# Performance work log

Hardware: AMD Instinct MI355X
Metric: run time of the kernel (lower is better)

Reference implementation:

```python
import jax, jax.numpy as jnp
import numpy as np
import math

BATCH, SEQ, D_MODEL, HEADS = 2, 2048, 1024, 16
DK = D_MODEL // HEADS  # 64
THETA = 10000.0


def _init_linear(key, d_in, d_out):
    std = math.sqrt(2.0 / (d_in + d_out))
    return (jax.random.truncated_normal(key, -3.0, 3.0, (d_in, d_out), jnp.float32) * std)


def setup_inputs() -> dict:
    key = jax.random.key(0)
    kx, kq, kk, kv, ko = jax.random.split(key, 5)
    x = jax.random.normal(kx, (BATCH, SEQ, D_MODEL), jnp.float32)
    W_Q = _init_linear(kq, D_MODEL, D_MODEL)
    W_K = _init_linear(kk, D_MODEL, D_MODEL)
    W_V = _init_linear(kv, D_MODEL, D_MODEL)
    W_O = _init_linear(ko, D_MODEL, D_MODEL)
    token_positions = jnp.arange(SEQ, dtype=jnp.int64 if jax.config.jax_enable_x64 else jnp.int32)
    # RoPE tables: angle[i, k] = i / theta**(2k/d_k), shape [max_seq_len, d_k//2]
    pos = jnp.arange(SEQ, dtype=jnp.float32)[:, None]
    inv_freq = THETA ** (-2.0 * jnp.arange(DK // 2, dtype=jnp.float32) / DK)
    angles = pos * inv_freq
    return {
        "x": x,
        "token_positions": token_positions,
        "W_Q": W_Q,
        "W_K": W_K,
        "W_V": W_V,
        "W_O": W_O,
        "cos": jnp.cos(angles),
        "sin": jnp.sin(angles),
    }


def _apply_rope(t, cos_p, sin_p):
    # t: [B, H, S, DK]; cos_p/sin_p: [S, DK//2] (already gathered by position)
    t_even = t[..., 0::2]
    t_odd = t[..., 1::2]
    even_rot = cos_p * t_even - sin_p * t_odd
    odd_rot = sin_p * t_even + cos_p * t_odd
    # interleave back: [..., DK//2, 2] -> [..., DK]
    return jnp.stack([even_rot, odd_rot], axis=-1).reshape(t.shape)


def reference(x, token_positions, W_Q, W_K, W_V, W_O, cos, sin):
    B, S, D = x.shape
    H, dk = HEADS, D // HEADS
    # QKV projections, split into heads: [B, S, D] -> [B, H, S, dk]
    def proj(W):
        return jnp.einsum("bsd,de->bse", x, W).reshape(B, S, H, dk).transpose(0, 2, 1, 3)
    Q, K, V = proj(W_Q), proj(W_K), proj(W_V)
    cos_p = cos[token_positions]  # [S, dk//2]
    sin_p = sin[token_positions]
    Q = _apply_rope(Q, cos_p, sin_p)
    K = _apply_rope(K, cos_p, sin_p)
    scores = jnp.einsum("bhqd,bhkd->bhqk", Q, K) / jnp.sqrt(jnp.asarray(dk, x.dtype))
    causal = jnp.tril(jnp.ones((S, S), dtype=bool))
    scores = jnp.where(causal, scores, -jnp.inf)
    attn = jax.nn.softmax(scores, axis=-1)
    out = jnp.einsum("bhqk,bhkd->bhqd", attn, V)  # [B, H, S, dk]
    out = out.transpose(0, 2, 1, 3).reshape(B, S, D)
    return jnp.einsum("bsd,de->bse", out, W_O)
```

## Files before the change

kernel.cpp:

```cpp
#include <hip/hip_runtime.h>

typedef unsigned short u16;
typedef unsigned int   u32;
typedef __bf16  bf16x8 __attribute__((ext_vector_type(8)));
typedef float   f32x4  __attribute__((ext_vector_type(4)));
typedef u32     u32x4  __attribute__((ext_vector_type(4)));

#define SEQ    2048
#define HEADS  16
#define DM     1024
#define NBH    32
#define NBS    4096

__device__ __forceinline__ u16 f2b(float f) {
    u32 x;
    __builtin_memcpy(&x, &f, 4);
    return (u16)((x + 0x7fffu + ((x >> 16) & 1u)) >> 16);
}

__device__ __forceinline__ u32 pk2(float lo, float hi) {
    return (u32)f2b(lo) | ((u32)f2b(hi) << 16);
}

__device__ __forceinline__ u32 pkc(float lo, float hi) {
    __bf16 a = (__bf16)lo, b = (__bf16)hi;
    u16 x, y;
    __builtin_memcpy(&x, &a, 2);
    __builtin_memcpy(&y, &b, 2);
    return (u32)x | ((u32)y << 16);
}

__device__ __forceinline__ bf16x8 ld_bf8(const u16* p) {
    return *(const bf16x8*)p;
}
__device__ __forceinline__ bf16x8 ld_f32x8_cvt(const float* p) {
    f32x4 a = *(const f32x4*)p;
    f32x4 b = *(const f32x4*)(p + 4);
    bf16x8 r;
    r[0] = (__bf16)a[0]; r[1] = (__bf16)a[1]; r[2] = (__bf16)a[2]; r[3] = (__bf16)a[3];
    r[4] = (__bf16)b[0]; r[5] = (__bf16)b[1]; r[6] = (__bf16)b[2]; r[7] = (__bf16)b[3];
    return r;
}

__global__ __launch_bounds__(256) void transpose_wqkv(const float* __restrict__ Wq,
                                                      const float* __restrict__ Wk,
                                                      const float* __restrict__ Wv,
                                                      u16* __restrict__ WqkvT) {
    __shared__ u16 tile[64][65];
    const int z  = blockIdx.z;
    const float* src = (z == 0) ? Wq : (z == 1) ? Wk : Wv;
    const int k0 = blockIdx.x * 64, n0 = blockIdx.y * 64;
    const int tid = threadIdx.x;
    for (int i = 0; i < 16; ++i) {
        int e = i * 256 + tid;
        int r = e >> 6, c = e & 63;
        tile[r][c] = f2b(src[(size_t)(k0 + r) * DM + n0 + c]);
    }
    __syncthreads();
    u16* dst = WqkvT + (size_t)z * DM * DM;
    for (int i = 0; i < 16; ++i) {
        int e = i * 256 + tid;
        int r = e >> 6, c = e & 63;
        dst[(size_t)(n0 + r) * DM + k0 + c] = tile[c][r];
    }
}

__global__ __launch_bounds__(256) void transpose_wo(const float* __restrict__ Wo,
                                                    u16* __restrict__ WoT) {
    __shared__ u16 tile[64][65];
    const int k0 = blockIdx.x * 64, n0 = blockIdx.y * 64;
    const int tid = threadIdx.x;
    for (int i = 0; i < 16; ++i) {
        int e = i * 256 + tid;
        int r = e >> 6, c = e & 63;
        tile[r][c] = f2b(Wo[(size_t)(k0 + r) * DM + n0 + c]);
    }
    __syncthreads();
    for (int i = 0; i < 16; ++i) {
        int e = i * 256 + tid;
        int r = e >> 6, c = e & 63;
        WoT[(size_t)(n0 + r) * DM + k0 + c] = tile[c][r];
    }
}

#define GEMM_BODY(A_EXPR, B_EXPR, K)                                                \
    __shared__ __attribute__((aligned(16))) __bf16 As[128 * 64];                    \
    __shared__ __attribute__((aligned(16))) __bf16 Bs[128 * 64];                    \
    const int tid  = threadIdx.x;                                                   \
    const int wave = tid >> 6, lane = tid & 63;                                     \
    const int quad = lane >> 4, col = lane & 15;                                    \
    const int wm = wave >> 1, wn = wave & 1;                                        \
    const int m0 = blockIdx.x * 128, n0 = blockIdx.y * 128;                         \
    const int srow = tid >> 3;                                           \
    const int scol = (tid & 7) * 8;                                      \
    f32x4 zero = {0.f, 0.f, 0.f, 0.f};                                              \
    f32x4 acc[4][4];                                                                \
    for (int i = 0; i < 4; ++i)                                                     \
        for (int j = 0; j < 4; ++j) acc[i][j] = zero;                               \
    for (int k0 = 0; k0 < (K); k0 += 64) {                                          \
        bf16x8 av[4], bv[4];                                                        \
        for (int p = 0; p < 4; ++p) {                                               \
            int row = p * 32 + srow;                                                \
            av[p] = A_EXPR;                                                         \
            bv[p] = B_EXPR;                                                         \
        }                                                                           \
        __syncthreads();                                                            \
        for (int p = 0; p < 4; ++p) {                                               \
            int row = p * 32 + srow;                                                \
            *(bf16x8*)&As[row * 64 + scol] = av[p];                                 \
            *(bf16x8*)&Bs[row * 64 + scol] = bv[p];                                 \
        }                                                                           \
        __syncthreads();                                                            \
        for (int ks = 0; ks < 2; ++ks) {                                            \
            bf16x8 af[4], bfr[4];                                                   \
            for (int mt = 0; mt < 4; ++mt)                                          \
                af[mt] = *(const bf16x8*)&As[(wm * 64 + mt * 16 + col) * 64 +       \
                                             ks * 32 + quad * 8];                   \
            for (int nt = 0; nt < 4; ++nt)                                          \
                bfr[nt] = *(const bf16x8*)&Bs[(wn * 64 + nt * 16 + col) * 64 +      \
                                              ks * 32 + quad * 8];                  \
            for (int mt = 0; mt < 4; ++mt)                                          \
                for (int nt = 0; nt < 4; ++nt)                                      \
                    acc[mt][nt] = __builtin_amdgcn_mfma_f32_16x16x32_bf16(          \
                        af[mt], bfr[nt], acc[mt][nt], 0, 0, 0);                     \
        }                                                                           \
    }

__global__ __launch_bounds__(256) void gemm_qkv(const float* __restrict__ Af,
                                                const u16* __restrict__ Bt,
                                                u16* __restrict__ Qp,
                                                u16* __restrict__ Kp,
                                                u16* __restrict__ Vt) {
    GEMM_BODY(ld_f32x8_cvt(Af + (size_t)(m0 + row) * DM + k0 + scol),
              ld_bf8(Bt + (size_t)(n0 + row) * DM + k0 + scol), DM)
    for (int mt = 0; mt < 4; ++mt)
        for (int nt = 0; nt < 4; ++nt) {
            int cc = n0 + wn * 64 + nt * 16 + col;
            int which = cc >> 10;
            int c1 = cc & 1023;
            int h = c1 >> 6, d = c1 & 63;
            for (int r = 0; r < 4; ++r) {
                int row = m0 + wm * 64 + mt * 16 + quad * 4 + r;
                int b = row >> 11, s = row & (SEQ - 1);
                u16 val = f2b(acc[mt][nt][r]);
                size_t bh = (size_t)(b * HEADS + h);
                if (which == 0)
                    Qp[(bh * SEQ + s) * 64 + d] = val;
                else if (which == 1)
                    Kp[(bh * SEQ + s) * 64 + d] = val;
                else
                    Vt[(bh * 64 + d) * SEQ + s] = val;
            }
        }
}

__global__ __launch_bounds__(256) void gemm_wo(const u16* __restrict__ A,
                                               const u16* __restrict__ Bt,
                                               float* __restrict__ C) {
    GEMM_BODY(ld_bf8(A + (size_t)(m0 + row) * DM + k0 + scol),
              ld_bf8(Bt + (size_t)(n0 + row) * DM + k0 + scol), DM)
    for (int mt = 0; mt < 4; ++mt)
        for (int nt = 0; nt < 4; ++nt)
            for (int r = 0; r < 4; ++r) {
                int row = m0 + wm * 64 + mt * 16 + quad * 4 + r;
                int cc  = n0 + wn * 64 + nt * 16 + col;
                C[(size_t)row * DM + cc] = acc[mt][nt][r];
            }
}

__global__ __launch_bounds__(256) void rope_qk(u16* __restrict__ Qp,
                                               u16* __restrict__ Kp,
                                               const float* __restrict__ cosT,
                                               const float* __restrict__ sinT) {
    int t = blockIdx.x * 256 + threadIdx.x;
    int p  = t & 31;
    int s  = (t >> 5) & (SEQ - 1);
    int hh = (t >> 16) & (HEADS - 1);
    int b  = t >> 20;

    float cv = cosT[s * 32 + p];
    float sv = sinT[s * 32 + p];

    size_t addr = (((size_t)(b * HEADS + hh)) * SEQ + s) * 64 + 2 * p;
    u32 q2 = *(const u32*)(Qp + addr);
    u32 k2 = *(const u32*)(Kp + addr);
    u32 qe_b = (q2 & 0xffff) << 16, qo_b = q2 & 0xffff0000u;
    u32 ke_b = (k2 & 0xffff) << 16, ko_b = k2 & 0xffff0000u;
    float qe, qo, ke, ko;
    __builtin_memcpy(&qe, &qe_b, 4); __builtin_memcpy(&qo, &qo_b, 4);
    __builtin_memcpy(&ke, &ke_b, 4); __builtin_memcpy(&ko, &ko_b, 4);

    u32 qout = (u32)f2b(0.125f * (cv * qe - sv * qo)) |
               ((u32)f2b(0.125f * (sv * qe + cv * qo)) << 16);
    u32 kout = (u32)f2b(cv * ke - sv * ko) | ((u32)f2b(sv * ke + cv * ko) << 16);
    *(u32*)(Qp + addr) = qout;
    *(u32*)(Kp + addr) = kout;
}

__global__ __launch_bounds__(256, 3) void flash_attn(const u16* __restrict__ Qp,
                                                     const u16* __restrict__ Kp,
                                                     const u16* __restrict__ Vt,
                                                     u16* __restrict__ O) {
    __shared__ float os[4][32][68];
    __shared__ float mM[4][32];
    __shared__ float mL[4][32];
    const int tid  = threadIdx.x;
    const int wave = tid >> 6, lane = tid & 63;
    const int quad = lane >> 4, col = lane & 15;
    const bool hi5 = lane >= 32;
    const bool hi4 = (lane & 16) != 0;
    const int bh = blockIdx.x;
    const int b = bh >> 4, h = bh & 15;
    const int qt = 63 - blockIdx.y;
    const int q0 = qt * 32;

    const u16* Qb = Qp + (size_t)bh * SEQ * 64;
    const u16* Kb = Kp + (size_t)bh * SEQ * 64;
    const u16* Vb = Vt + (size_t)bh * 64 * SEQ;

    bf16x8 bq00 = ld_bf8(Qb + (size_t)(q0 + col) * 64 + quad * 8);
    bf16x8 bq01 = ld_bf8(Qb + (size_t)(q0 + col) * 64 + 32 + quad * 8);
    bf16x8 bq10 = ld_bf8(Qb + (size_t)(q0 + 16 + col) * 64 + quad * 8);
    bf16x8 bq11 = ld_bf8(Qb + (size_t)(q0 + 16 + col) * 64 + 32 + quad * 8);

    f32x4 zero = {0.f, 0.f, 0.f, 0.f};
    f32x4 o0[4] = {zero, zero, zero, zero};
    f32x4 o1[4] = {zero, zero, zero, zero};
    float m0_ = -1e30f, m1_ = -1e30f;
    float lp0 = 0.f, lp1 = 0.f;

    const int nkt = qt + 1;
    int kt = wave;
    bf16x8 ck00, ck01, ck10, ck11;
    if (kt < nkt) {
        const int kb = kt << 5;
        ck00 = ld_bf8(Kb + (size_t)(kb + col) * 64 + quad * 8);
        ck01 = ld_bf8(Kb + (size_t)(kb + col) * 64 + 32 + quad * 8);
        ck10 = ld_bf8(Kb + (size_t)(kb + 16 + col) * 64 + quad * 8);
        ck11 = ld_bf8(Kb + (size_t)(kb + 16 + col) * 64 + 32 + quad * 8);
    }

    for (; kt < nkt; kt += 4) {
        const int kb = kt << 5;
        bf16x8 bv0 = ld_bf8(Vb + (size_t)(0 * 16 + col) * SEQ + kb + quad * 8);
        bf16x8 bv1 = ld_bf8(Vb + (size_t)(1 * 16 + col) * SEQ + kb + quad * 8);
        bf16x8 bv2 = ld_bf8(Vb + (size_t)(2 * 16 + col) * SEQ + kb + quad * 8);
        bf16x8 bv3 = ld_bf8(Vb + (size_t)(3 * 16 + col) * SEQ + kb + quad * 8);
        int kn = kt + 4; if (kn >= nkt) kn = kt;
        const int kb2 = kn << 5;
        bf16x8 nk00 = ld_bf8(Kb + (size_t)(kb2 + col) * 64 + quad * 8);
        bf16x8 nk01 = ld_bf8(Kb + (size_t)(kb2 + col) * 64 + 32 + quad * 8);
        bf16x8 nk10 = ld_bf8(Kb + (size_t)(kb2 + 16 + col) * 64 + quad * 8);
        bf16x8 nk11 = ld_bf8(Kb + (size_t)(kb2 + 16 + col) * 64 + 32 + quad * 8);

        f32x4 s00 = zero, s01 = zero, s10 = zero, s11 = zero;
        s00 = __builtin_amdgcn_mfma_f32_16x16x32_bf16(ck00, bq00, s00, 0, 0, 0);
        s10 = __builtin_amdgcn_mfma_f32_16x16x32_bf16(ck00, bq10, s10, 0, 0, 0);
        s00 = __builtin_amdgcn_mfma_f32_16x16x32_bf16(ck01, bq01, s00, 0, 0, 0);
        s10 = __builtin_amdgcn_mfma_f32_16x16x32_bf16(ck01, bq11, s10, 0, 0, 0);
        s01 = __builtin_amdgcn_mfma_f32_16x16x32_bf16(ck10, bq00, s01, 0, 0, 0);
        s11 = __builtin_amdgcn_mfma_f32_16x16x32_bf16(ck10, bq10, s11, 0, 0, 0);
        s01 = __builtin_amdgcn_mfma_f32_16x16x32_bf16(ck11, bq01, s01, 0, 0, 0);
        s11 = __builtin_amdgcn_mfma_f32_16x16x32_bf16(ck11, bq11, s11, 0, 0, 0);

        float v00[4], v01[4], v10[4], v11[4];
        float lm0 = -1e30f, lm1 = -1e30f;
        if (kt == qt) {
            for (int r = 0; r < 4; ++r) {
                int krel = quad * 4 + r;
                float a0 = (krel > col) ? -1e30f : s00[r];
                float b0 = -1e30f;
                float a1 = s10[r];
                float b1 = (krel > col) ? -1e30f : s11[r];
                v00[r] = a0; v01[r] = b0; v10[r] = a1; v11[r] = b1;
                lm0 = fmaxf(lm0, fmaxf(a0, b0));
                lm1 = fmaxf(lm1, fmaxf(a1, b1));
            }
        } else {
            for (int r = 0; r < 4; ++r) {
                v00[r] = s00[r]; v01[r] = s01[r];
                v10[r] = s10[r]; v11[r] = s11[r];
                lm0 = fmaxf(lm0, fmaxf(v00[r], v01[r]));
                lm1 = fmaxf(lm1, fmaxf(v10[r], v11[r]));
            }
        }

        float dd = fmaxf(lm0 - m0_, lm1 - m1_);
        if (__any(dd > 8.f)) {
            float lr0 = fmaxf(lm0, __shfl_xor(lm0, 16));
            lr0 = fmaxf(lr0, __shfl_xor(lr0, 32));
            float lr1 = fmaxf(lm1, __shfl_xor(lm1, 16));
            lr1 = fmaxf(lr1, __shfl_xor(lr1, 32));
            float mn0 = fmaxf(m0_, lr0), mn1 = fmaxf(m1_, lr1);
            float al0 = __expf(m0_ - mn0), al1 = __expf(m1_ - mn1);
            m0_ = mn0; m1_ = mn1;
            lp0 *= al0; lp1 *= al1;
            for (int r = 0; r < 4; ++r) {
                float ar0 = __shfl(al0, quad * 4 + r);
                float ar1 = __shfl(al1, quad * 4 + r);
                for (int nt = 0; nt < 4; ++nt) {
                    o0[nt][r] *= ar0;
                    o1[nt][r] *= ar1;
                }
            }
        }

        for (int r = 0; r < 4; ++r) {
            v00[r] = __expf(v00[r] - m0_);
            v01[r] = __expf(v01[r] - m0_);
            v10[r] = __expf(v10[r] - m1_);
            v11[r] = __expf(v11[r] - m1_);
            lp0 += v00[r] + v01[r];
            lp1 += v10[r] + v11[r];
        }

        u32 fwa0[4], fwa1[4];
        {
            u32 A0 = pkc(v00[0], v00[1]), A1 = pkc(v00[2], v00[3]);
            u32 B0 = pkc(v01[0], v01[1]), B1 = pkc(v01[2], v01[3]);
            u32 g0 = hi5 ? A0 : B0,  g1 = hi5 ? A1 : B1;
            u32 r0 = __shfl_xor(g0, 32), r1 = __shfl_xor(g1, 32);
            u32 P00 = hi5 ? r0 : A0,  P01 = hi5 ? r1 : A1;
            u32 P10 = hi5 ? B0 : r0,  P11 = hi5 ? B1 : r1;
            u32 h0 = hi4 ? P00 : P10, h1 = hi4 ? P01 : P11;
            u32 u0 = __shfl_xor(h0, 16), u1 = __shfl_xor(h1, 16);
            fwa0[0] = hi4 ? u0 : P00;  fwa0[1] = hi4 ? u1 : P01;
            fwa0[2] = hi4 ? P10 : u0;  fwa0[3] = hi4 ? P11 : u1;
        }
        {
            u32 A0 = pkc(v10[0], v10[1]), A1 = pkc(v10[2], v10[3]);
            u32 B0 = pkc(v11[0], v11[1]), B1 = pkc(v11[2], v11[3]);
            u32 g0 = hi5 ? A0 : B0,  g1 = hi5 ? A1 : B1;
            u32 r0 = __shfl_xor(g0, 32), r1 = __shfl_xor(g1, 32);
            u32 P00 = hi5 ? r0 : A0,  P01 = hi5 ? r1 : A1;
            u32 P10 = hi5 ? B0 : r0,  P11 = hi5 ? B1 : r1;
            u32 h0 = hi4 ? P00 : P10, h1 = hi4 ? P01 : P11;
            u32 u0 = __shfl_xor(h0, 16), u1 = __shfl_xor(h1, 16);
            fwa1[0] = hi4 ? u0 : P00;  fwa1[1] = hi4 ? u1 : P01;
            fwa1[2] = hi4 ? P10 : u0;  fwa1[3] = hi4 ? P11 : u1;
        }
        bf16x8 pf0, pf1;
        __builtin_memcpy(&pf0, fwa0, 16);
        __builtin_memcpy(&pf1, fwa1, 16);

        o0[0] = __builtin_amdgcn_mfma_f32_16x16x32_bf16(pf0, bv0, o0[0], 0, 0, 0);
        o1[0] = __builtin_amdgcn_mfma_f32_16x16x32_bf16(pf1, bv0, o1[0], 0, 0, 0);
        o0[1] = __builtin_amdgcn_mfma_f32_16x16x32_bf16(pf0, bv1, o0[1], 0, 0, 0);
        o1[1] = __builtin_amdgcn_mfma_f32_16x16x32_bf16(pf1, bv1, o1[1], 0, 0, 0);
        o0[2] = __builtin_amdgcn_mfma_f32_16x16x32_bf16(pf0, bv2, o0[2], 0, 0, 0);
        o1[2] = __builtin_amdgcn_mfma_f32_16x16x32_bf16(pf1, bv2, o1[2], 0, 0, 0);
        o0[3] = __builtin_amdgcn_mfma_f32_16x16x32_bf16(pf0, bv3, o0[3], 0, 0, 0);
        o1[3] = __builtin_amdgcn_mfma_f32_16x16x32_bf16(pf1, bv3, o1[3], 0, 0, 0);

        ck00 = nk00; ck01 = nk01; ck10 = nk10; ck11 = nk11;
    }

    float lt0 = lp0;
    lt0 += __shfl_xor(lt0, 16); lt0 += __shfl_xor(lt0, 32);
    float lt1 = lp1;
    lt1 += __shfl_xor(lt1, 16); lt1 += __shfl_xor(lt1, 32);
    if (quad == 0) {
        mM[wave][col] = m0_;      mL[wave][col] = lt0;
        mM[wave][16 + col] = m1_; mL[wave][16 + col] = lt1;
    }
    for (int nt = 0; nt < 4; ++nt)
        for (int r = 0; r < 4; ++r) {
            os[wave][quad * 4 + r][nt * 16 + col]      = o0[nt][r];
            os[wave][16 + quad * 4 + r][nt * 16 + col] = o1[nt][r];
        }
    __syncthreads();

    {
        const int q  = tid >> 3;
        const int d0 = (tid & 7) * 8;
        float M = fmaxf(fmaxf(mM[0][q], mM[1][q]), fmaxf(mM[2][q], mM[3][q]));
        float L = 0.f;
        f32x4 a0 = {0.f, 0.f, 0.f, 0.f}, a1 = {0.f, 0.f, 0.f, 0.f};
        for (int w = 0; w < 4; ++w) {
            float e = __expf(mM[w][q] - M);
            L += e * mL[w][q];
            f32x4 p0 = *(const f32x4*)&os[w][q][d0];
            f32x4 p1 = *(const f32x4*)&os[w][q][d0 + 4];
            for (int j = 0; j < 4; ++j) { a0[j] += e * p0[j]; a1[j] += e * p1[j]; }
        }
        float inv = 1.f / L;
        u32x4 val;
        val[0] = pk2(a0[0] * inv, a0[1] * inv);
        val[1] = pk2(a0[2] * inv, a0[3] * inv);
        val[2] = pk2(a1[0] * inv, a1[1] * inv);
        val[3] = pk2(a1[2] * inv, a1[3] * inv);
        *(u32x4*)&O[((size_t)b * SEQ + q0 + q) * DM + h * 64 + d0] = val;
    }
}

extern "C" void kernel_launch(void* const* d_in, const int* in_sizes, int n_in,
                              void* d_out, int out_size, void* d_ws, size_t ws_size,
                              hipStream_t stream) {
    const float* x    = (const float*)d_in[0];
    const float* Wq   = (const float*)d_in[2];
    const float* Wk   = (const float*)d_in[3];
    const float* Wv   = (const float*)d_in[4];
    const float* Wo   = (const float*)d_in[5];
    const float* cosT = (const float*)d_in[6];
    const float* sinT = (const float*)d_in[7];
    float* out = (float*)d_out;

    u16* ws    = (u16*)d_ws;
    u16* qp    = ws;
    u16* kp    = ws + 4194304;
    u16* vt    = ws + 8388608;
    u16* woT   = ws + 8388608;
    u16* wqkvT = ws + 12582912;
    u16* ao    = ws + 12582912;

    dim3 blk(256);
    transpose_wqkv<<<dim3(16, 16, 3), blk, 0, stream>>>(Wq, Wk, Wv, wqkvT);
    gemm_qkv<<<dim3(32, 24), blk, 0, stream>>>(x, wqkvT, qp, kp, vt);
    rope_qk<<<dim3(8192), blk, 0, stream>>>(qp, kp, cosT, sinT);
    flash_attn<<<dim3(NBH, 64), blk, 0, stream>>>(qp, kp, vt, ao);
    transpose_wo<<<dim3(16, 16), blk, 0, stream>>>(Wo, woT);
    gemm_wo<<<dim3(32, 8), blk, 0, stream>>>(ao, woT, out);
}
```

Measured before the change: 247.7 us.

## Use direct global-to-LDS loads with XOR swizzle in GEMMs and vectorize RoPE

Replaces the GEMM macro with explicit kernels that load bf16 tiles straight into LDS via global_load_lds and use an XOR-swizzled LDS layout to avoid bank conflicts on fragment reads. In gemm_qkv the fp32 activation tile for the next k-step is prefetched into registers while the current step computes. The RoPE kernel now processes 8 elements per thread with 128-bit loads and stores instead of 2. This cuts register staging and LDS conflicts, but the swizzle index math must stay consistent between writes and reads, and the direct-to-LDS path depends on the compiler builtin's semantics.

```diff
diff --git a/kernel.cpp b/kernel.cpp
--- a/kernel.cpp
+++ b/kernel.cpp
@@ -40,6 +40,13 @@
     r[0] = (__bf16)a[0]; r[1] = (__bf16)a[1]; r[2] = (__bf16)a[2]; r[3] = (__bf16)a[3];
     r[4] = (__bf16)b[0]; r[5] = (__bf16)b[1]; r[6] = (__bf16)b[2]; r[7] = (__bf16)b[3];
     return r;
+}
+
+__device__ __forceinline__ void gl_lds16(const u16* g, __bf16* l) {
+    __builtin_amdgcn_global_load_lds(
+        (__attribute__((address_space(1))) void*)g,
+        (__attribute__((address_space(3))) void*)l,
+        16, 0, 0);
 }
 
 __global__ __launch_bounds__(256) void transpose_wqkv(const float* __restrict__ Wq,
@@ -83,56 +90,67 @@
     }
 }
 
-#define GEMM_BODY(A_EXPR, B_EXPR, K)                                                \
-    __shared__ __attribute__((aligned(16))) __bf16 As[128 * 64];                    \
-    __shared__ __attribute__((aligned(16))) __bf16 Bs[128 * 64];                    \
-    const int tid  = threadIdx.x;                                                   \
-    const int wave = tid >> 6, lane = tid & 63;                                     \
-    const int quad = lane >> 4, col = lane & 15;                                    \
-    const int wm = wave >> 1, wn = wave & 1;                                        \
-    const int m0 = blockIdx.x * 128, n0 = blockIdx.y * 128;                         \
-    const int srow = tid >> 3;                                           \
-    const int scol = (tid & 7) * 8;                                      \
-    f32x4 zero = {0.f, 0.f, 0.f, 0.f};                                              \
-    f32x4 acc[4][4];                                                                \
-    for (int i = 0; i < 4; ++i)                                                     \
-        for (int j = 0; j < 4; ++j) acc[i][j] = zero;                               \
-    for (int k0 = 0; k0 < (K); k0 += 64) {                                          \
-        bf16x8 av[4], bv[4];                                                        \
-        for (int p = 0; p < 4; ++p) {                                               \
-            int row = p * 32 + srow;                                                \
-            av[p] = A_EXPR;                                                         \
-            bv[p] = B_EXPR;                                                         \
-        }                                                                           \
-        __syncthreads();                                                            \
-        for (int p = 0; p < 4; ++p) {                                               \
-            int row = p * 32 + srow;                                                \
-            *(bf16x8*)&As[row * 64 + scol] = av[p];                                 \
-            *(bf16x8*)&Bs[row * 64 + scol] = bv[p];                                 \
-        }                                                                           \
-        __syncthreads();                                                            \
-        for (int ks = 0; ks < 2; ++ks) {                                            \
-            bf16x8 af[4], bfr[4];                                                   \
-            for (int mt = 0; mt < 4; ++mt)                                          \
-                af[mt] = *(const bf16x8*)&As[(wm * 64 + mt * 16 + col) * 64 +       \
-                                             ks * 32 + quad * 8];                   \
-            for (int nt = 0; nt < 4; ++nt)                                          \
-                bfr[nt] = *(const bf16x8*)&Bs[(wn * 64 + nt * 16 + col) * 64 +      \
-                                              ks * 32 + quad * 8];                  \
-            for (int mt = 0; mt < 4; ++mt)                                          \
-                for (int nt = 0; nt < 4; ++nt)                                      \
-                    acc[mt][nt] = __builtin_amdgcn_mfma_f32_16x16x32_bf16(          \
-                        af[mt], bfr[nt], acc[mt][nt], 0, 0, 0);                     \
-        }                                                                           \
-    }
 
 __global__ __launch_bounds__(256) void gemm_qkv(const float* __restrict__ Af,
                                                 const u16* __restrict__ Bt,
                                                 u16* __restrict__ Qp,
                                                 u16* __restrict__ Kp,
                                                 u16* __restrict__ Vt) {
-    GEMM_BODY(ld_f32x8_cvt(Af + (size_t)(m0 + row) * DM + k0 + scol),
-              ld_bf8(Bt + (size_t)(n0 + row) * DM + k0 + scol), DM)
+    __shared__ __attribute__((aligned(16))) __bf16 As[128 * 64];
+    __shared__ __attribute__((aligned(16))) __bf16 Bs[128 * 64];
+    const int tid  = threadIdx.x;
+    const int wave = tid >> 6, lane = tid & 63;
+    const int quad = lane >> 4, col = lane & 15;
+    const int wm = wave >> 1, wn = wave & 1;
+    const int m0 = blockIdx.x * 128, n0 = blockIdx.y * 128;
+    const int srow = tid >> 3;
+    const int sc8  = (tid & 7) * 8;
+    const int aslot = (((tid & 7) ^ (srow & 7)) << 3);
+    const int c7 = col & 7;
+
+    f32x4 zero = {0.f, 0.f, 0.f, 0.f};
+    f32x4 acc[4][4];
+    for (int i = 0; i < 4; ++i)
+        for (int j = 0; j < 4; ++j) acc[i][j] = zero;
+
+    bf16x8 av[4];
+#pragma unroll
+    for (int p = 0; p < 4; ++p)
+        av[p] = ld_f32x8_cvt(Af + (size_t)(m0 + p * 32 + srow) * DM + sc8);
+
+    for (int k0 = 0; k0 < DM; k0 += 64) {
+        __syncthreads();
+#pragma unroll
+        for (int p = 0; p < 4; ++p)
+            gl_lds16(Bt + (size_t)(n0 + p * 32 + srow) * DM + k0 + aslot,
+                     &Bs[p * 2048 + tid * 8]);
+#pragma unroll
+        for (int p = 0; p < 4; ++p)
+            *(bf16x8*)&As[(p * 32 + srow) * 64 + aslot] = av[p];
+        __syncthreads();
+        int kn = k0 + 64; if (kn >= DM) kn = k0;
+#pragma unroll
+        for (int p = 0; p < 4; ++p)
+            av[p] = ld_f32x8_cvt(Af + (size_t)(m0 + p * 32 + srow) * DM + kn + sc8);
+#pragma unroll
+        for (int ks = 0; ks < 2; ++ks) {
+            const int rsl = ((((ks << 2) | quad) ^ c7) << 3);
+            bf16x8 af[4], bfr[4];
+#pragma unroll
+            for (int mt = 0; mt < 4; ++mt)
+                af[mt] = *(const bf16x8*)&As[(wm * 64 + mt * 16 + col) * 64 + rsl];
+#pragma unroll
+            for (int nt = 0; nt < 4; ++nt)
+                bfr[nt] = *(const bf16x8*)&Bs[(wn * 64 + nt * 16 + col) * 64 + rsl];
+#pragma unroll
+            for (int mt = 0; mt < 4; ++mt)
+#pragma unroll
+                for (int nt = 0; nt < 4; ++nt)
+                    acc[mt][nt] = __builtin_amdgcn_mfma_f32_16x16x32_bf16(
+                        af[mt], bfr[nt], acc[mt][nt], 0, 0, 0);
+        }
+    }
+
     for (int mt = 0; mt < 4; ++mt)
         for (int nt = 0; nt < 4; ++nt) {
             int cc = n0 + wn * 64 + nt * 16 + col;
@@ -157,8 +175,52 @@
 __global__ __launch_bounds__(256) void gemm_wo(const u16* __restrict__ A,
                                                const u16* __restrict__ Bt,
                                                float* __restrict__ C) {
-    GEMM_BODY(ld_bf8(A + (size_t)(m0 + row) * DM + k0 + scol),
-              ld_bf8(Bt + (size_t)(n0 + row) * DM + k0 + scol), DM)
+    __shared__ __attribute__((aligned(16))) __bf16 As[128 * 64];
+    __shared__ __attribute__((aligned(16))) __bf16 Bs[128 * 64];
+    const int tid  = threadIdx.x;
+    const int wave = tid >> 6, lane = tid & 63;
+    const int quad = lane >> 4, col = lane & 15;
+    const int wm = wave >> 1, wn = wave & 1;
+    const int m0 = blockIdx.x * 128, n0 = blockIdx.y * 128;
+    const int srow = tid >> 3;
+    const int aslot = (((tid & 7) ^ (srow & 7)) << 3);
+    const int c7 = col & 7;
+
+    f32x4 zero = {0.f, 0.f, 0.f, 0.f};
+    f32x4 acc[4][4];
+    for (int i = 0; i < 4; ++i)
+        for (int j = 0; j < 4; ++j) acc[i][j] = zero;
+
+    for (int k0 = 0; k0 < DM; k0 += 64) {
+        __syncthreads();
+#pragma unroll
+        for (int p = 0; p < 4; ++p)
+            gl_lds16(A + (size_t)(m0 + p * 32 + srow) * DM + k0 + aslot,
+                     &As[p * 2048 + tid * 8]);
+#pragma unroll
+        for (int p = 0; p < 4; ++p)
+            gl_lds16(Bt + (size_t)(n0 + p * 32 + srow) * DM + k0 + aslot,
+                     &Bs[p * 2048 + tid * 8]);
+        __syncthreads();
+#pragma unroll
+        for (int ks = 0; ks < 2; ++ks) {
+            const int rsl = ((((ks << 2) | quad) ^ c7) << 3);
+            bf16x8 af[4], bfr[4];
+#pragma unroll
+            for (int mt = 0; mt < 4; ++mt)
+                af[mt] = *(const bf16x8*)&As[(wm * 64 + mt * 16 + col) * 64 + rsl];
+#pragma unroll
+            for (int nt = 0; nt < 4; ++nt)
+                bfr[nt] = *(const bf16x8*)&Bs[(wn * 64 + nt * 16 + col) * 64 + rsl];
+#pragma unroll
+            for (int mt = 0; mt < 4; ++mt)
+#pragma unroll
+                for (int nt = 0; nt < 4; ++nt)
+                    acc[mt][nt] = __builtin_amdgcn_mfma_f32_16x16x32_bf16(
+                        af[mt], bfr[nt], acc[mt][nt], 0, 0, 0);
+        }
+    }
+
     for (int mt = 0; mt < 4; ++mt)
         for (int nt = 0; nt < 4; ++nt)
             for (int r = 0; r < 4; ++r) {
@@ -173,28 +235,33 @@
                                                const float* __restrict__ cosT,
                                                const float* __restrict__ sinT) {
     int t = blockIdx.x * 256 + threadIdx.x;
-    int p  = t & 31;
-    int s  = (t >> 5) & (SEQ - 1);
-    int hh = (t >> 16) & (HEADS - 1);
-    int b  = t >> 20;
-
-    float cv = cosT[s * 32 + p];
-    float sv = sinT[s * 32 + p];
-
-    size_t addr = (((size_t)(b * HEADS + hh)) * SEQ + s) * 64 + 2 * p;
-    u32 q2 = *(const u32*)(Qp + addr);
-    u32 k2 = *(const u32*)(Kp + addr);
-    u32 qe_b = (q2 & 0xffff) << 16, qo_b = q2 & 0xffff0000u;
-    u32 ke_b = (k2 & 0xffff) << 16, ko_b = k2 & 0xffff0000u;
-    float qe, qo, ke, ko;
-    __builtin_memcpy(&qe, &qe_b, 4); __builtin_memcpy(&qo, &qo_b, 4);
-    __builtin_memcpy(&ke, &ke_b, 4); __builtin_memcpy(&ko, &ko_b, 4);
-
-    u32 qout = (u32)f2b(0.125f * (cv * qe - sv * qo)) |
-               ((u32)f2b(0.125f * (sv * qe + cv * qo)) << 16);
-    u32 kout = (u32)f2b(cv * ke - sv * ko) | ((u32)f2b(sv * ke + cv * ko) << 16);
-    *(u32*)(Qp + addr) = qout;
-    *(u32*)(Kp + addr) = kout;
+    int g  = t & 7;
+    int s  = (t >> 3) & (SEQ - 1);
+    int hh = (t >> 14) & (HEADS - 1);
+    int b  = t >> 18;
+
+    f32x4 cv = *(const f32x4*)&cosT[s * 32 + g * 4];
+    f32x4 sv = *(const f32x4*)&sinT[s * 32 + g * 4];
+
+    size_t addr = (((size_t)(b * HEADS + hh)) * SEQ + s) * 64 + g * 8;
+    u32x4 q4 = *(const u32x4*)(Qp + addr);
+    u32x4 k4 = *(const u32x4*)(Kp + addr);
+    u32x4 qo4, ko4;
+#pragma unroll
+    for (int j = 0; j < 4; ++j) {
+        u32 q2 = q4[j], k2 = k4[j];
+        u32 qe_b = (q2 & 0xffff) << 16, qo_b = q2 & 0xffff0000u;
+        u32 ke_b = (k2 & 0xffff) << 16, ko_b = k2 & 0xffff0000u;
+        float qe, qo, ke, ko;
+        __builtin_memcpy(&qe, &qe_b, 4); __builtin_memcpy(&qo, &qo_b, 4);
+        __builtin_memcpy(&ke, &ke_b, 4); __builtin_memcpy(&ko, &ko_b, 4);
+        qo4[j] = (u32)f2b(0.125f * (cv[j] * qe - sv[j] * qo)) |
+                 ((u32)f2b(0.125f * (sv[j] * qe + cv[j] * qo)) << 16);
+        ko4[j] = (u32)f2b(cv[j] * ke - sv[j] * ko) |
+                 ((u32)f2b(sv[j] * ke + cv[j] * ko) << 16);
+    }
+    *(u32x4*)(Qp + addr) = qo4;
+    *(u32x4*)(Kp + addr) = ko4;
 }
 
 __global__ __launch_bounds__(256, 3) void flash_attn(const u16* __restrict__ Qp,
@@ -416,7 +483,7 @@
     dim3 blk(256);
     transpose_wqkv<<<dim3(16, 16, 3), blk, 0, stream>>>(Wq, Wk, Wv, wqkvT);
     gemm_qkv<<<dim3(32, 24), blk, 0, stream>>>(x, wqkvT, qp, kp, vt);
-    rope_qk<<<dim3(8192), blk, 0, stream>>>(qp, kp, cosT, sinT);
+    rope_qk<<<dim3(2048), blk, 0, stream>>>(qp, kp, cosT, sinT);
     flash_attn<<<dim3(NBH, 64), blk, 0, stream>>>(qp, kp, vt, ao);
     transpose_wo<<<dim3(16, 16), blk, 0, stream>>>(Wo, woT);
     gemm_wo<<<dim3(32, 8), blk, 0, stream>>>(ao, woT, out);
```

Result: no change. 245.3 us (-1.0%).
